# Optimization experiments

Measured on AMD Instinct MI355X. Metric: run time of the kernel, lower is better.

The kernel has to match this reference:

```python
import jax, jax.numpy as jnp
import numpy as np

B, N, D = 2, 2048, 1024
H = 16
HD = D // H


def setup_inputs() -> dict:
    key = jax.random.key(0)
    ks = jax.random.split(key, 10)
    s = 1.0 / np.sqrt(D)
    return {
        "x": jax.random.normal(ks[0], (B, N, D), dtype=jnp.float32),
        "B_gaussian": jax.random.normal(ks[1], (B, N, N), dtype=jnp.float32),
        "Wq": jax.random.normal(ks[2], (D, D), dtype=jnp.float32) * s,
        "bq": jnp.zeros((D,), dtype=jnp.float32),
        "Wk": jax.random.normal(ks[3], (D, D), dtype=jnp.float32) * s,
        "bk": jnp.zeros((D,), dtype=jnp.float32),
        "Wv": jax.random.normal(ks[4], (D, D), dtype=jnp.float32) * s,
        "bv": jnp.zeros((D,), dtype=jnp.float32),
        "Wo": jax.random.normal(ks[5], (D, D), dtype=jnp.float32) * s,
        "bo": jnp.zeros((D,), dtype=jnp.float32),
        "lam": jnp.float32(0.5),
    }


def reference(x, B_gaussian, Wq, bq, Wk, bk, Wv, bv, Wo, bo, lam):
    b, n, d = x.shape
    # project and split heads: [b, h, n, hd]
    def heads(W, bias):
        return (x @ W + bias).reshape(b, n, H, HD).transpose(0, 2, 1, 3)
    q = heads(Wq, bq)
    k = heads(Wk, bk)
    v = heads(Wv, bv)
    scale = 1.0 / np.sqrt(HD)
    # scores [b, h, n, n] with Gaussian bias broadcast across heads
    scores = jnp.einsum("bhid,bhjd->bhij", q, k) * scale + lam * B_gaussian[:, None, :, :]
    w = jax.nn.softmax(scores, axis=-1)
    out = jnp.einsum("bhij,bhjd->bhid", w, v)
    out = out.transpose(0, 2, 1, 3).reshape(b, n, d)
    return out @ Wo + bo
```

## Files before the change

kernel.cpp:

```cpp
#include <hip/hip_runtime.h>
#include <math.h>
#include <stdint.h>

namespace {
constexpr int kB  = 2;
constexpr int kN  = 2048;
constexpr int kD  = 1024;
constexpr int kH  = 16;
constexpr int kM  = kB * kN;
}

typedef __attribute__((ext_vector_type(8))) _Float16 f16x8;
typedef __attribute__((ext_vector_type(2))) __fp16   fp16x2;
typedef __attribute__((ext_vector_type(4))) float    f32x4;

__device__ __forceinline__ void split16(float v, _Float16& h, _Float16& l) {
    h = (_Float16)v;
    l = (_Float16)(v - (float)h);
}

__device__ __forceinline__ void gl2lds16(const _Float16* g, _Float16* l) {
    __builtin_amdgcn_global_load_lds(
        (const __attribute__((address_space(1))) void*)g,
        (__attribute__((address_space(3))) void*)l, 16, 0, 0);
}

__global__ __launch_bounds__(256)
void cvt16(const float* __restrict__ x, _Float16* __restrict__ o)
{
    const size_t i = ((size_t)blockIdx.x * 256 + threadIdx.x) * 8;
    const float4 a = *(const float4*)(x + i);
    const float4 b = *(const float4*)(x + i + 4);
    _Float16 h[8] = {(_Float16)a.x, (_Float16)a.y, (_Float16)a.z, (_Float16)a.w,
                     (_Float16)b.x, (_Float16)b.y, (_Float16)b.z, (_Float16)b.w};
    *(uint4*)(o + i) = *(uint4*)h;
}

__global__ __launch_bounds__(256)
void bgprep(const float* __restrict__ Bg, const float* __restrict__ lam_p,
            _Float16* __restrict__ bgC)
{
    const int t    = blockIdx.x * 256 + threadIdx.x;
    const int lane = t & 63;
    const int i16  = (t >> 6) & 127;
    const int jt   = (t >> 13) & 31;
    const int b    = t >> 18;
    const int q    = lane >> 4;
    const int m    = lane & 15;
    const float c  = lam_p[0] * 8.0f;
    const float* src = Bg + ((size_t)b * kN + i16 * 16 + m) * kN + jt * 64 + q * 4;
    _Float16 h[16];
#pragma unroll
    for (int js = 0; js < 4; ++js) {
        const float4 v = *(const float4*)(src + js * 16);
        h[js * 4 + 0] = (_Float16)(c * v.x);
        h[js * 4 + 1] = (_Float16)(c * v.y);
        h[js * 4 + 2] = (_Float16)(c * v.z);
        h[js * 4 + 3] = (_Float16)(c * v.w);
    }
    _Float16* dst = bgC + (size_t)t * 16;
    *(uint4*)(dst)     = *(uint4*)(h);
    *(uint4*)(dst + 8) = *(uint4*)(h + 8);
}

__global__ __launch_bounds__(256)
void wcvt_t(const float* __restrict__ W, _Float16* __restrict__ Ot)
{
    __shared__ float sT[64][69];
    const int tid = threadIdx.x;
    const int k0 = blockIdx.x << 6;
    const int n0 = blockIdx.y << 6;
#pragma unroll
    for (int rep = 0; rep < 4; ++rep) {
        const int idx = tid + (rep << 8);
        const int kr  = idx >> 4;
        const int c4  = (idx & 15) << 2;
        const float4 v = *(const float4*)(W + (size_t)(k0 + kr) * kD + n0 + c4);
        sT[kr][c4 + 0] = v.x; sT[kr][c4 + 1] = v.y;
        sT[kr][c4 + 2] = v.z; sT[kr][c4 + 3] = v.w;
    }
    __syncthreads();
#pragma unroll
    for (int rep = 0; rep < 2; ++rep) {
        const int slot = tid + (rep << 8);
        const int n  = slot >> 3;
        const int k8 = (slot & 7) << 3;
        _Float16 h8[8];
#pragma unroll
        for (int j = 0; j < 8; ++j) h8[j] = (_Float16)sT[k8 + j][n];
        *(uint4*)(Ot + (size_t)(n0 + n) * kD + k0 + k8) = *(uint4*)h8;
    }
}

__global__ __launch_bounds__(256)
void wsplit_t(const float* __restrict__ W, _Float16* __restrict__ Oh,
              _Float16* __restrict__ Ol)
{
    __shared__ float sT[64][69];
    const int tid = threadIdx.x;
    const int k0 = blockIdx.x << 6;
    const int n0 = blockIdx.y << 6;
#pragma unroll
    for (int rep = 0; rep < 4; ++rep) {
        const int idx = tid + (rep << 8);
        const int kr  = idx >> 4;
        const int c4  = (idx & 15) << 2;
        const float4 v = *(const float4*)(W + (size_t)(k0 + kr) * kD + n0 + c4);
        sT[kr][c4 + 0] = v.x; sT[kr][c4 + 1] = v.y;
        sT[kr][c4 + 2] = v.z; sT[kr][c4 + 3] = v.w;
    }
    __syncthreads();
#pragma unroll
    for (int rep = 0; rep < 2; ++rep) {
        const int slot = tid + (rep << 8);
        const int n  = slot >> 3;
        const int k8 = (slot & 7) << 3;
        _Float16 h8[8], l8[8];
#pragma unroll
        for (int j = 0; j < 8; ++j) split16(sT[k8 + j][n], h8[j], l8[j]);
        *(uint4*)(Oh + (size_t)(n0 + n) * kD + k0 + k8) = *(uint4*)h8;
        *(uint4*)(Ol + (size_t)(n0 + n) * kD + k0 + k8) = *(uint4*)l8;
    }
}

__global__ __launch_bounds__(256)
void gemm16(const _Float16* __restrict__ A, const _Float16* __restrict__ Bt,
            const _Float16* __restrict__ Btl,
            const float* __restrict__ b0, const float* __restrict__ b1,
            const float* __restrict__ b2,
            _Float16* __restrict__ Qf, _Float16* __restrict__ Kf,
            _Float16* __restrict__ Vt, float* __restrict__ outF, int mode)
{
    extern __shared__ _Float16 dyn[];
    _Float16* sA  = dyn;
    _Float16* sB  = dyn + 128 * 64;
    _Float16* sBl = dyn + 2 * 128 * 64;

    const int tid  = threadIdx.x;
    const int lane = tid & 63;
    const int w    = tid >> 6;
    const int quad = lane >> 4;
    const int m16  = lane & 15;
    const int wrow = (w >> 1) << 6;
    const int wcol = (w & 1) << 6;

    const int row0 = blockIdx.y << 7;
    const int col0 = blockIdx.x << 7;

    f32x4 acc[4][4];
#pragma unroll
    for (int mr = 0; mr < 4; ++mr)
#pragma unroll
        for (int nr = 0; nr < 4; ++nr) acc[mr][nr] = (f32x4){0.f, 0.f, 0.f, 0.f};

    const int srl = lane >> 3;
    const int sg  = lane & 7;

    auto stage = [&](const _Float16* gsrc, _Float16* ldst) {
#pragma unroll
        for (int t = 0; t < 4; ++t) {
            const int rr = (w << 5) + (t << 3);
            const int r  = rr + srl;
            const int gg = (sg ^ (r & 7)) << 3;
            gl2lds16(gsrc + (size_t)r * kD + gg, ldst + rr * 64);
        }
    };

    for (int kt = 0; kt < 16; ++kt) {
        const int k0 = kt << 6;
        stage(A  + (size_t)row0 * kD + k0, sA);
        stage(Bt + (size_t)col0 * kD + k0, sB);
        if (mode == 1) stage(Btl + (size_t)col0 * kD + k0, sBl);
        __syncthreads();

#pragma unroll
        for (int ks = 0; ks < 2; ++ks) {
            const int sw = (((ks << 2) | quad) ^ (m16 & 7)) << 3;
            f16x8 af[4], bf[4], blf[4];
#pragma unroll
            for (int mr = 0; mr < 4; ++mr)
                af[mr] = *(const f16x8*)(sA + (wrow + mr * 16 + m16) * 64 + sw);
#pragma unroll
            for (int nr = 0; nr < 4; ++nr) {
                const int off = (wcol + nr * 16 + m16) * 64 + sw;
                bf[nr] = *(const f16x8*)(sB + off);
                if (mode == 1) blf[nr] = *(const f16x8*)(sBl + off);
            }
#pragma unroll
            for (int mr = 0; mr < 4; ++mr)
#pragma unroll
                for (int nr = 0; nr < 4; ++nr) {
                    acc[mr][nr] = __builtin_amdgcn_mfma_f32_16x16x32_f16(af[mr], bf[nr], acc[mr][nr], 0, 0, 0);
                    if (mode == 1)
                        acc[mr][nr] = __builtin_amdgcn_mfma_f32_16x16x32_f16(af[mr], blf[nr], acc[mr][nr], 0, 0, 0);
                }
        }
        __syncthreads();
    }

    if (mode == 1) {
#pragma unroll
        for (int mr = 0; mr < 4; ++mr)
#pragma unroll
            for (int nr = 0; nr < 4; ++nr)
#pragma unroll
                for (int r = 0; r < 4; ++r) {
                    const int row = row0 + wrow + mr * 16 + quad * 4 + r;
                    const int col = col0 + wcol + nr * 16 + m16;
                    outF[(size_t)row * kD + col] = acc[mr][nr][r] + b0[col];
                }
        return;
    }

    const float* bias; int cb; _Float16* dst = nullptr; bool vmode = false;
    if (col0 < 1024)      { bias = b0; cb = col0;        dst = Qf; }
    else if (col0 < 2048) { bias = b1; cb = col0 - 1024; dst = Kf; }
    else                  { bias = b2; cb = col0 - 2048; vmode = true; }

    _Float16* T = dyn;

    if (!vmode) {
#pragma unroll
        for (int mr = 0; mr < 4; ++mr)
#pragma unroll
            for (int nr = 0; nr < 4; ++nr)
#pragma unroll
                for (int r = 0; r < 4; ++r) {
                    const int row = wrow + mr * 16 + quad * 4 + r;
                    const int cl  = wcol + nr * 16 + m16;
                    T[row * 136 + cl] = (_Float16)(acc[mr][nr][r] + bias[cb + cl]);
                }
        __syncthreads();
#pragma unroll
        for (int rep = 0; rep < 8; ++rep) {
            const int slot = tid + (rep << 8);
            const int row = slot >> 4;
            const int c8  = (slot & 15) << 3;
            *(uint4*)(dst + (size_t)(row0 + row) * kD + cb + c8) =
                *(const uint4*)(T + row * 136 + c8);
        }
    } else {
#pragma unroll
        for (int mr = 0; mr < 4; ++mr)
#pragma unroll
            for (int nr = 0; nr < 4; ++nr)
#pragma unroll
                for (int r = 0; r < 4; ++r) {
                    const int tok = wrow + mr * 16 + quad * 4 + r;
                    const int cl  = wcol + nr * 16 + m16;
                    T[cl * 136 + tok] = (_Float16)(acc[mr][nr][r] + bias[cb + cl]);
                }
        __syncthreads();
        const int b  = row0 >> 11;
        const int n0 = row0 & (kN - 1);
#pragma unroll
        for (int rep = 0; rep < 8; ++rep) {
            const int slot = tid + (rep << 8);
            const int cl = slot >> 4;
            const int t8 = (slot & 15) << 3;
            *(uint4*)(Vt + ((size_t)(b * kD + cb + cl)) * kN + n0 + t8) =
                *(const uint4*)(T + cl * 136 + t8);
        }
    }
}

__global__ __launch_bounds__(512)
void attn_f16(const _Float16* __restrict__ Qf, const _Float16* __restrict__ Kf,
              const _Float16* __restrict__ Vt, const _Float16* __restrict__ BgC,
              _Float16* __restrict__ AOh)
{
    __shared__ _Float16 sK[64][72];
    __shared__ _Float16 sV[64][72];
    __shared__ _Float16 sP[8][16][72];

    const int tid  = threadIdx.x;
    const int lane = tid & 63;
    const int w    = tid >> 6;
    const int quad = lane >> 4;
    const int m16  = lane & 15;

    const int qt = blockIdx.x;
    const int bh = blockIdx.y;
    const int b  = bh >> 4;
    const int h  = bh & 15;
    const int i0 = qt << 7;

    f16x8 qf[2];
    {
        const size_t qoff = (size_t)(b * kN + i0 + w * 16 + m16) * kD + h * 64 + quad * 8;
        qf[0] = *(const f16x8*)(Qf + qoff);
        qf[1] = *(const f16x8*)(Qf + qoff + 32);
    }

    f32x4 O[4];
#pragma unroll
    for (int ds = 0; ds < 4; ++ds) O[ds] = (f32x4){0.f, 0.f, 0.f, 0.f};
    float lsum = 0.f;

    const int krow = tid >> 3;
    const int kc8  = (tid & 7) << 3;

    const _Float16* bgbase =
        BgC + (((size_t)b * 32 * 128 + (qt * 8 + w)) * 64 + lane) * 16;
    constexpr size_t kBgJt = (size_t)128 * 64 * 16;

    uint4 kp, vp;
    f16x8 bg0, bg1;
    auto loadTile = [&](int jt) {
        const int j0 = jt << 6;
        kp = *(const uint4*)(Kf + (size_t)(b * kN + j0 + krow) * kD + h * 64 + kc8);
        vp = *(const uint4*)(Vt + (size_t)(b * kD + h * 64 + krow) * kN + j0 + kc8);
        const _Float16* bp = bgbase + (size_t)jt * kBgJt;
        bg0 = *(const f16x8*)(bp);
        bg1 = *(const f16x8*)(bp + 8);
    };

    loadTile(0);

    for (int jt = 0; jt < kN / 64; ++jt) {
        __syncthreads();
        *(uint4*)&sK[krow][kc8] = kp;
        *(uint4*)&sV[krow][kc8] = vp;
        __syncthreads();

        f32x4 sacc[4];
#pragma unroll
        for (int r = 0; r < 4; ++r) {
            sacc[0][r] = (float)bg0[r];
            sacc[1][r] = (float)bg0[4 + r];
            sacc[2][r] = (float)bg1[r];
            sacc[3][r] = (float)bg1[4 + r];
        }

        if (jt < kN / 64 - 1) loadTile(jt + 1);

#pragma unroll
        for (int ks = 0; ks < 2; ++ks)
#pragma unroll
            for (int js = 0; js < 4; ++js) {
                const f16x8 kf = *(const f16x8*)&sK[js * 16 + m16][ks * 32 + quad * 8];
                sacc[js] = __builtin_amdgcn_mfma_f32_16x16x32_f16(kf, qf[ks], sacc[js], 0, 0, 0);
            }

#pragma unroll
        for (int js = 0; js < 4; ++js) {
            float p[4];
#pragma unroll
            for (int r = 0; r < 4; ++r)
                p[r] = __expf(fmaf(sacc[js][r], 0.125f, -4.0f));
            lsum += (p[0] + p[1]) + (p[2] + p[3]);
            union { fp16x2 h[2]; uint2 u; } pk;
            pk.h[0] = __builtin_amdgcn_cvt_pkrtz(p[0], p[1]);
            pk.h[1] = __builtin_amdgcn_cvt_pkrtz(p[2], p[3]);
            *(uint2*)&sP[w][m16][js * 16 + quad * 4] = pk.u;
        }
        __asm__ volatile("s_waitcnt lgkmcnt(0)" ::: "memory");

#pragma unroll
        for (int ks = 0; ks < 2; ++ks) {
            const f16x8 pf = *(const f16x8*)&sP[w][m16][ks * 32 + quad * 8];
#pragma unroll
            for (int ds = 0; ds < 4; ++ds) {
                const f16x8 vf = *(const f16x8*)&sV[ds * 16 + m16][ks * 32 + quad * 8];
                O[ds] = __builtin_amdgcn_mfma_f32_16x16x32_f16(pf, vf, O[ds], 0, 0, 0);
            }
        }
    }

    float l = lsum;
    l += __shfl_xor(l, 16, 64);
    l += __shfl_xor(l, 32, 64);

    const int orow = b * kN + i0 + w * 16 + quad * 4;
#pragma unroll
    for (int r = 0; r < 4; ++r) {
        const float inv = 1.0f / __shfl(l, quad * 4 + r, 64);
#pragma unroll
        for (int ds = 0; ds < 4; ++ds)
            AOh[(size_t)(orow + r) * kD + h * 64 + ds * 16 + m16] =
                (_Float16)(O[ds][r] * inv);
    }
}

extern "C" void kernel_launch(void* const* d_in, const int* in_sizes, int n_in,
                              void* d_out, int out_size, void* d_ws, size_t ws_size,
                              hipStream_t stream)
{
    (void)in_sizes; (void)n_in; (void)out_size; (void)ws_size;

    const float* x   = (const float*)d_in[0];
    const float* Bg  = (const float*)d_in[1];
    const float* Wq  = (const float*)d_in[2];
    const float* bq  = (const float*)d_in[3];
    const float* Wk  = (const float*)d_in[4];
    const float* bk  = (const float*)d_in[5];
    const float* Wv  = (const float*)d_in[6];
    const float* bv  = (const float*)d_in[7];
    const float* Wo  = (const float*)d_in[8];
    const float* bo  = (const float*)d_in[9];
    const float* lam = (const float*)d_in[10];
    float* out = (float*)d_out;
    _Float16* ws16 = (_Float16*)d_ws;

    constexpr size_t kQKV = (size_t)kM * kD;
    constexpr size_t kW   = (size_t)kD * kD;
    _Float16* Qf   = ws16;
    _Float16* Kf   = ws16 + 1 * kQKV;
    _Float16* Vt   = ws16 + 2 * kQKV;
    _Float16* x16  = ws16 + 3 * kQKV;
    _Float16* AOh  = x16;
    _Float16* Wt3  = ws16 + 4 * kQKV;
    _Float16* Woth = Wt3 + 3 * kW;
    _Float16* Wotl = Woth + kW;
    _Float16* BgC  = Wotl + kW;

    dim3 blk(256);

    cvt16<<<dim3(2048), blk, 0, stream>>>(x, x16);
    bgprep<<<dim3(2048), blk, 0, stream>>>(Bg, lam, BgC);
    dim3 wg(kD / 64, kD / 64);
    wcvt_t  <<<wg, blk, 0, stream>>>(Wq, Wt3);
    wcvt_t  <<<wg, blk, 0, stream>>>(Wk, Wt3 + kW);
    wcvt_t  <<<wg, blk, 0, stream>>>(Wv, Wt3 + 2 * kW);
    wsplit_t<<<wg, blk, 0, stream>>>(Wo, Woth, Wotl);

    gemm16<<<dim3(3 * kD / 128, kM / 128), blk, 34816, stream>>>(
        x16, Wt3, nullptr, bq, bk, bv, Qf, Kf, Vt, nullptr, 0);

    attn_f16<<<dim3(kN / 128, kB * kH), dim3(512), 0, stream>>>(
        Qf, Kf, Vt, BgC, AOh);

    gemm16<<<dim3(kD / 128, kM / 128), blk, 49152, stream>>>(
        AOh, Woth, Wotl, bo, nullptr, nullptr,
        nullptr, nullptr, nullptr, out, 1);
}
```

Measured before the change: 262.7 us.

## Keep softmax P in registers and double-buffer K/V tiles in attention

The V-transpose writeback permutes token order within each 64-token tile so that the MFMA accumulator layout of P matches the B-operand layout. P can then be packed directly into registers instead of round-tripping through shared memory. The attention loop double-buffers K/V in LDS so each tile needs one barrier instead of two. It also adds s_setprio around the MFMA bursts and a launch-bounds occupancy hint. The risks are higher register pressure and a tight coupling between the projection kernel's layout and the attention kernel's fragment indexing.

```diff
diff --git a/kernel.cpp b/kernel.cpp
--- a/kernel.cpp
+++ b/kernel.cpp
@@ -246,9 +246,12 @@
             for (int nr = 0; nr < 4; ++nr)
 #pragma unroll
                 for (int r = 0; r < 4; ++r) {
-                    const int tok = wrow + mr * 16 + quad * 4 + r;
-                    const int cl  = wcol + nr * 16 + m16;
-                    T[cl * 136 + tok] = (_Float16)(acc[mr][nr][r] + bias[cb + cl]);
+                    const int tok  = wrow + mr * 16 + quad * 4 + r;
+                    const int tokP = (tok & 64) | (tok & 32) |
+                                     (((tok >> 2) & 3) << 3) |
+                                     (((tok >> 4) & 1) << 2) | (tok & 3);
+                    const int cl   = wcol + nr * 16 + m16;
+                    T[cl * 136 + tokP] = (_Float16)(acc[mr][nr][r] + bias[cb + cl]);
                 }
         __syncthreads();
         const int b  = row0 >> 11;
@@ -264,14 +267,13 @@
     }
 }
 
-__global__ __launch_bounds__(512)
+__global__ __launch_bounds__(512, 4)
 void attn_f16(const _Float16* __restrict__ Qf, const _Float16* __restrict__ Kf,
               const _Float16* __restrict__ Vt, const _Float16* __restrict__ BgC,
               _Float16* __restrict__ AOh)
 {
-    __shared__ _Float16 sK[64][72];
-    __shared__ _Float16 sV[64][72];
-    __shared__ _Float16 sP[8][16][72];
+    __shared__ _Float16 sK[2][64][72];
+    __shared__ _Float16 sV[2][64][72];
 
     const int tid  = threadIdx.x;
     const int lane = tid & 63;
@@ -304,44 +306,37 @@
         BgC + (((size_t)b * 32 * 128 + (qt * 8 + w)) * 64 + lane) * 16;
     constexpr size_t kBgJt = (size_t)128 * 64 * 16;
 
-    uint4 kp, vp;
-    f16x8 bg0, bg1;
-    auto loadTile = [&](int jt) {
+    auto loadT = [&](int jt, uint4& kp, uint4& vp, f16x8& g0, f16x8& g1) {
         const int j0 = jt << 6;
         kp = *(const uint4*)(Kf + (size_t)(b * kN + j0 + krow) * kD + h * 64 + kc8);
         vp = *(const uint4*)(Vt + (size_t)(b * kD + h * 64 + krow) * kN + j0 + kc8);
         const _Float16* bp = bgbase + (size_t)jt * kBgJt;
-        bg0 = *(const f16x8*)(bp);
-        bg1 = *(const f16x8*)(bp + 8);
+        g0 = *(const f16x8*)(bp);
+        g1 = *(const f16x8*)(bp + 8);
     };
 
-    loadTile(0);
-
-    for (int jt = 0; jt < kN / 64; ++jt) {
-        __syncthreads();
-        *(uint4*)&sK[krow][kc8] = kp;
-        *(uint4*)&sV[krow][kc8] = vp;
-        __syncthreads();
-
+    auto phaseCompute = [&](const _Float16 (&Kt)[64][72],
+                            const _Float16 (&Vs)[64][72],
+                            const f16x8& g0, const f16x8& g1) {
         f32x4 sacc[4];
 #pragma unroll
         for (int r = 0; r < 4; ++r) {
-            sacc[0][r] = (float)bg0[r];
-            sacc[1][r] = (float)bg0[4 + r];
-            sacc[2][r] = (float)bg1[r];
-            sacc[3][r] = (float)bg1[4 + r];
-        }
-
-        if (jt < kN / 64 - 1) loadTile(jt + 1);
-
+            sacc[0][r] = (float)g0[r];
+            sacc[1][r] = (float)g0[4 + r];
+            sacc[2][r] = (float)g1[r];
+            sacc[3][r] = (float)g1[4 + r];
+        }
+        __builtin_amdgcn_s_setprio(1);
 #pragma unroll
         for (int ks = 0; ks < 2; ++ks)
 #pragma unroll
             for (int js = 0; js < 4; ++js) {
-                const f16x8 kf = *(const f16x8*)&sK[js * 16 + m16][ks * 32 + quad * 8];
+                const f16x8 kf = *(const f16x8*)&Kt[js * 16 + m16][ks * 32 + quad * 8];
                 sacc[js] = __builtin_amdgcn_mfma_f32_16x16x32_f16(kf, qf[ks], sacc[js], 0, 0, 0);
             }
-
+        __builtin_amdgcn_s_setprio(0);
+
+        union { f16x8 v; unsigned u[4]; } pf[2];
 #pragma unroll
         for (int js = 0; js < 4; ++js) {
             float p[4];
@@ -349,22 +344,48 @@
             for (int r = 0; r < 4; ++r)
                 p[r] = __expf(fmaf(sacc[js][r], 0.125f, -4.0f));
             lsum += (p[0] + p[1]) + (p[2] + p[3]);
-            union { fp16x2 h[2]; uint2 u; } pk;
-            pk.h[0] = __builtin_amdgcn_cvt_pkrtz(p[0], p[1]);
-            pk.h[1] = __builtin_amdgcn_cvt_pkrtz(p[2], p[3]);
-            *(uint2*)&sP[w][m16][js * 16 + quad * 4] = pk.u;
-        }
-        __asm__ volatile("s_waitcnt lgkmcnt(0)" ::: "memory");
-
-#pragma unroll
-        for (int ks = 0; ks < 2; ++ks) {
-            const f16x8 pf = *(const f16x8*)&sP[w][m16][ks * 32 + quad * 8];
+            const fp16x2 lo = __builtin_amdgcn_cvt_pkrtz(p[0], p[1]);
+            const fp16x2 hi = __builtin_amdgcn_cvt_pkrtz(p[2], p[3]);
+            union { fp16x2 h; unsigned u; } ua, ub;
+            ua.h = lo; ub.h = hi;
+            pf[js >> 1].u[(js & 1) * 2 + 0] = ua.u;
+            pf[js >> 1].u[(js & 1) * 2 + 1] = ub.u;
+        }
+
+        __builtin_amdgcn_s_setprio(1);
+#pragma unroll
+        for (int ks = 0; ks < 2; ++ks)
 #pragma unroll
             for (int ds = 0; ds < 4; ++ds) {
-                const f16x8 vf = *(const f16x8*)&sV[ds * 16 + m16][ks * 32 + quad * 8];
-                O[ds] = __builtin_amdgcn_mfma_f32_16x16x32_f16(pf, vf, O[ds], 0, 0, 0);
+                const f16x8 vf = *(const f16x8*)&Vs[ds * 16 + m16][ks * 32 + quad * 8];
+                O[ds] = __builtin_amdgcn_mfma_f32_16x16x32_f16(pf[ks].v, vf, O[ds], 0, 0, 0);
             }
-        }
+        __builtin_amdgcn_s_setprio(0);
+    };
+
+    uint4 kp0, vp0, kp1, vp1;
+    f16x8 bgA0, bgA1, bgB0, bgB1;
+
+    loadT(0, kp0, vp0, bgA0, bgA1);
+    *(uint4*)&sK[0][krow][kc8] = kp0;
+    *(uint4*)&sV[0][krow][kc8] = vp0;
+    loadT(1, kp1, vp1, bgB0, bgB1);
+    __syncthreads();
+
+    for (int t = 0; t < kN / 64; t += 2) {
+        phaseCompute(sK[0], sV[0], bgA0, bgA1);
+        if (t + 2 < kN / 64) loadT(t + 2, kp0, vp0, bgA0, bgA1);
+        *(uint4*)&sK[1][krow][kc8] = kp1;
+        *(uint4*)&sV[1][krow][kc8] = vp1;
+        __syncthreads();
+
+        phaseCompute(sK[1], sV[1], bgB0, bgB1);
+        if (t + 3 < kN / 64) loadT(t + 3, kp1, vp1, bgB0, bgB1);
+        if (t + 2 < kN / 64) {
+            *(uint4*)&sK[0][krow][kc8] = kp0;
+            *(uint4*)&sV[0][krow][kc8] = vp0;
+        }
+        __syncthreads();
     }
 
     float l = lsum;
```

After: 260.3 us. Within noise of the previous version (-0.9%).
